# Kernel tuning notes

Measured on AMD Instinct MI355X. Metric: run time of the kernel, lower is better.

Reference implementation:

```python
import jax, jax.numpy as jnp
import numpy as np

H = 768
V = 21128
LN_EPS = 1e-12


def setup_inputs() -> dict:
    key = jax.random.key(0)
    ks = jax.random.split(key, 12)
    s = 0.02
    inp = {
        "cls_vec": jax.random.normal(ks[0], (8, H), dtype=jnp.float32),
        # LSTM (PyTorch layout: weight_ih (4H,H), weight_hh (4H,H), biases (4H,))
        "W_ih": s * jax.random.normal(ks[1], (4 * H, H), dtype=jnp.float32),
        "W_hh": s * jax.random.normal(ks[2], (4 * H, H), dtype=jnp.float32),
        "b_ih": s * jax.random.normal(ks[3], (4 * H,), dtype=jnp.float32),
        "b_hh": s * jax.random.normal(ks[4], (4 * H,), dtype=jnp.float32),
        # BertPredictionHeadTransform: dense(H,H) + gelu + LayerNorm
        "W_dense": s * jax.random.normal(ks[5], (H, H), dtype=jnp.float32),
        "b_dense": s * jax.random.normal(ks[6], (H,), dtype=jnp.float32),
        "ln_gamma": jnp.ones((H,), dtype=jnp.float32),
        "ln_beta": jnp.zeros((H,), dtype=jnp.float32),
        # decoder: Linear(H, V, bias=False) + separate bias param (tied)
        "W_voc": s * jax.random.normal(ks[7], (V, H), dtype=jnp.float32),
        "b_voc": jnp.zeros((V,), dtype=jnp.float32),
        "steps": 511,
    }
    return inp


def _lstm_cell(x, h, c, W_ih, W_hh, b_ih, b_hh):
    gates = x @ W_ih.T + b_ih + h @ W_hh.T + b_hh  # (B, 4H)
    i, f, g, o = jnp.split(gates, 4, axis=-1)
    i = jax.nn.sigmoid(i)
    f = jax.nn.sigmoid(f)
    g = jnp.tanh(g)
    o = jax.nn.sigmoid(o)
    c = f * c + i * g
    h = o * jnp.tanh(c)
    return h, c


def _head(x, W_dense, b_dense, ln_gamma, ln_beta, W_voc, b_voc):
    t = jax.nn.gelu(x @ W_dense.T + b_dense, approximate=False)
    mu = jnp.mean(t, axis=-1, keepdims=True)
    var = jnp.mean(jnp.square(t - mu), axis=-1, keepdims=True)
    t = (t - mu) * jax.lax.rsqrt(var + LN_EPS) * ln_gamma + ln_beta
    return t @ W_voc.T + b_voc  # (B, V)


def reference(cls_vec, W_ih, W_hh, b_ih, b_hh, W_dense, b_dense,
              ln_gamma, ln_beta, W_voc, b_voc, steps):
    B = cls_vec.shape[0]
    zeros = jnp.zeros((B, H), dtype=cls_vec.dtype)
    # decoder_out, (h_1, c_1) = self.decoder(cls_vec.unsqueeze(1))
    h, c = _lstm_cell(cls_vec, zeros, zeros, W_ih, W_hh, b_ih, b_hh)

    def step(carry, _):
        h, c = carry
        h, c = _lstm_cell(carry[0], h, c, W_ih, W_hh, b_ih, b_hh)
        logits = _head(h, W_dense, b_dense, ln_gamma, ln_beta, W_voc, b_voc)
        return (h, c), logits

    (h, c), logits = jax.lax.scan(step, (h, c), None, length=steps)
    return logits  # (steps, B, V)
```

## Files before the change

### kernel.cpp

```cpp
#include <hip/hip_runtime.h>
#include <hip/hip_bf16.h>
#include <cstdint>

#define HD 768
#define VOC 21128
#define VOCP 21248
#define NSTEPS 511
#define MROWS 4088
#define MPAD 4096
#define NBL 192

typedef float f32x4 __attribute__((ext_vector_type(4)));
typedef short short8 __attribute__((ext_vector_type(8)));

#define OFF_HW   768
#define OFF_HALL 49920
#define OFF_WDT  12632576ULL
#define OFF_T    14991872ULL
#define OFF_WV   21283328ULL
#define PADH 772

__device__ __forceinline__ unsigned short f2bf(float x) {
  unsigned u = __float_as_uint(x);
  u += 0x7FFFu + ((u >> 16) & 1u);
  return (unsigned short)(u >> 16);
}

__device__ __forceinline__ void gl_lds16(const void* g, void* l) {
  __builtin_amdgcn_global_load_lds(
      (const __attribute__((address_space(1))) void*)g,
      (__attribute__((address_space(3))) void*)l, 16, 0, 0);
}

__device__ __forceinline__ void st_u32(uint32_t* p, uint32_t v) {
  __hip_atomic_store(p, v, __ATOMIC_RELAXED, __HIP_MEMORY_SCOPE_AGENT);
}
__device__ __forceinline__ uint32_t ld_u32(const uint32_t* p) {
  return __hip_atomic_load(p, __ATOMIC_RELAXED, __HIP_MEMORY_SCOPE_AGENT);
}

__device__ __forceinline__ float swz8(float x) {
  return __int_as_float(__builtin_amdgcn_ds_swizzle(__float_as_int(x), 0x201F));
}
__device__ __forceinline__ float swz16(float x) {
  return __int_as_float(__builtin_amdgcn_ds_swizzle(__float_as_int(x), 0x401F));
}

__device__ __forceinline__ float sigf(float x) {
  return __builtin_amdgcn_rcpf(1.f + __expf(-x));
}
__device__ __forceinline__ float tanhf_fast(float x) {
  float ax = fabsf(x);
  float e = __expf(-2.f * ax);
  float t = (1.f - e) * __builtin_amdgcn_rcpf(1.f + e);
  return copysignf(t, x);
}

__global__ __launch_bounds__(256) void prep_kernel(
    const float* __restrict__ Wd, float* __restrict__ WdT,
    const float* __restrict__ Wv, unsigned short* __restrict__ WvB,
    uint32_t* __restrict__ hw) {
  unsigned idx = blockIdx.x * 256 + threadIdx.x;
  unsigned stride = gridDim.x * 256;
  for (unsigned i = idx; i < 12288; i += stride) hw[i] = 0;
  for (unsigned i = idx; i < HD * HD; i += stride) {
    unsigned k = i / HD, j = i - k * HD;
    WdT[i] = Wd[j * HD + k];
  }
  const unsigned NV = (unsigned)VOCP * HD, NVr = (unsigned)VOC * HD;
  for (unsigned i = idx; i < NV; i += stride)
    WvB[i] = f2bf(i < NVr ? Wv[i] : 0.f);
}

__global__ __launch_bounds__(256) void lstm_kernel(
    const float* __restrict__ cls, const float* __restrict__ Wih,
    const float* __restrict__ Whh, const float* __restrict__ bih,
    const float* __restrict__ bhh, uint32_t* __restrict__ hw,
    float* __restrict__ Hall) {
  __shared__ float h_lds[8 * PADH];
  __shared__ float red[4][2][16][8];
  __shared__ float sbias[16];
  const int t = threadIdx.x;
  const int blk = blockIdx.x;
  const int p_ = t & 7;
  const int s_ = t >> 3;
  const int ks = s_ * 24;
  const int r0 = 2 * p_, r1 = r0 + 1;
  const int grow0 = (r0 >> 2) * HD + blk * 4 + (r0 & 3);
  const int grow1 = (r1 >> 2) * HD + blk * 4 + (r1 & 3);
  float w0[24], w1[24];
#pragma unroll
  for (int j = 0; j < 24; ++j) {
    w0[j] = Wih[(size_t)grow0 * HD + ks + j];
    w1[j] = Wih[(size_t)grow1 * HD + ks + j];
  }
  if (t < 16) {
    int gr = (t >> 2) * HD + blk * 4 + (t & 3);
    sbias[t] = bih[gr] + bhh[gr];
  }
  float cstate = 0.f;
  const int lane = t & 63, wv = t >> 6, hf = (lane >> 5);

  auto do_step = [&](uint32_t* __restrict__ hw_out, int tag,
                     float* __restrict__ hall_row) {
    float acc0[8], acc1[8];
#pragma unroll
    for (int b = 0; b < 8; ++b) { acc0[b] = 0.f; acc1[b] = 0.f; }
#pragma unroll
    for (int b = 0; b < 8; ++b) {
      const float* hb = &h_lds[b * PADH + ks];
#pragma unroll
      for (int j4 = 0; j4 < 6; ++j4) {
        f32x4 hv = *reinterpret_cast<const f32x4*>(hb + j4 * 4);
#pragma unroll
        for (int e = 0; e < 4; ++e) {
          acc0[b] = fmaf(w0[j4 * 4 + e], hv[e], acc0[b]);
          acc1[b] = fmaf(w1[j4 * 4 + e], hv[e], acc1[b]);
        }
      }
    }
#pragma unroll
    for (int b = 0; b < 8; ++b) {
      acc0[b] += swz8(acc0[b]);  acc0[b] += swz16(acc0[b]);
      acc1[b] += swz8(acc1[b]);  acc1[b] += swz16(acc1[b]);
    }
    if ((lane & 31) < 8) {
#pragma unroll
      for (int b = 0; b < 8; ++b) {
        red[wv][hf][r0][b] = acc0[b];
        red[wv][hf][r1][b] = acc1[b];
      }
    }
    __syncthreads();
    if (t < 32) {
      int ul = t >> 3, b = t & 7;
      float gs[4];
#pragma unroll
      for (int g = 0; g < 4; ++g) {
        int r = g * 4 + ul;
        float s = sbias[r];
#pragma unroll
        for (int w2 = 0; w2 < 4; ++w2) s += red[w2][0][r][b] + red[w2][1][r][b];
        gs[g] = s;
      }
      float iv = sigf(gs[0]);
      float fv = sigf(gs[1]);
      float gv = tanhf_fast(gs[2]);
      float ov = sigf(gs[3]);
      cstate = fv * cstate + iv * gv;
      float hn = ov * tanhf_fast(cstate);
      union { _Float16 f; unsigned short u; } cv;
      cv.f = (_Float16)hn;
      st_u32(&hw_out[(blk * 4 + ul) * 8 + b],
             ((uint32_t)tag << 16) | (uint32_t)cv.u);
      if (hall_row) hall_row[(size_t)b * HD + blk * 4 + ul] = hn;
    }
  };

  for (int i = t; i < 1536; i += 256) {
    int b = i / 192, c4 = i - b * 192;
    *reinterpret_cast<f32x4*>(&h_lds[b * PADH + c4 * 4]) =
        reinterpret_cast<const f32x4*>(cls)[i];
  }
  __syncthreads();
  do_step(hw + 6144, 1, nullptr);
#pragma unroll
  for (int j = 0; j < 24; ++j) {
    w0[j] += Whh[(size_t)grow0 * HD + ks + j];
    w1[j] += Whh[(size_t)grow1 * HD + ks + j];
  }
  for (int s = 1; s <= NSTEPS; ++s) {
    const uint32_t* src = hw + (s & 1) * 6144;
    uint32_t w[24];
    bool ok;
    do {
      ok = true;
#pragma unroll
      for (int k = 0; k < 24; ++k) {
        w[k] = ld_u32(&src[t + k * 256]);
        if ((w[k] >> 16) != (uint32_t)s) ok = false;
      }
    } while (!ok);
#pragma unroll
    for (int k = 0; k < 24; ++k) {
      int f = t + k * 256;
      union { unsigned short u; _Float16 f16; } cv;
      cv.u = (unsigned short)(w[k] & 0xFFFFu);
      h_lds[(f & 7) * PADH + (f >> 3)] = (float)cv.f16;
    }
    __syncthreads();
    do_step(hw + ((s + 1) & 1) * 6144, s + 1,
            Hall + (size_t)(s - 1) * (8 * HD));
  }
}

__global__ __launch_bounds__(256) void head_kernel(
    const float* __restrict__ Hall, const float* __restrict__ WdT,
    const float* __restrict__ bd, const float* __restrict__ gamma,
    const float* __restrict__ beta, unsigned short* __restrict__ Tm) {
  __shared__ float hT[HD][16];
  __shared__ float rbuf[4][16];
  __shared__ float mu_s[16], rs_s[16];
  const int t = threadIdx.x;
  const int r0 = blockIdx.x * 16;
  {
    const int row = t & 15, ksl = t >> 4;
    const float* src = Hall + (size_t)(r0 + row) * HD + ksl * 48;
#pragma unroll
    for (int i = 0; i < 12; ++i) {
      f32x4 v = *reinterpret_cast<const f32x4*>(src + i * 4);
      int k = ksl * 48 + i * 4;
      hT[k][row] = v[0]; hT[k + 1][row] = v[1];
      hT[k + 2][row] = v[2]; hT[k + 3][row] = v[3];
    }
  }
  __syncthreads();
  float a0[16], a1[16], a2[16];
#pragma unroll
  for (int r = 0; r < 16; ++r) { a0[r] = 0.f; a1[r] = 0.f; a2[r] = 0.f; }
  for (int k = 0; k < HD; ++k) {
    float wa = WdT[(size_t)k * HD + t];
    float wb = WdT[(size_t)k * HD + t + 256];
    float wc = WdT[(size_t)k * HD + t + 512];
    f32x4 hv4[4];
#pragma unroll
    for (int q = 0; q < 4; ++q)
      hv4[q] = *reinterpret_cast<const f32x4*>(&hT[k][q * 4]);
#pragma unroll
    for (int r = 0; r < 16; ++r) {
      float hv = hv4[r >> 2][r & 3];
      a0[r] = fmaf(wa, hv, a0[r]);
      a1[r] = fmaf(wb, hv, a1[r]);
      a2[r] = fmaf(wc, hv, a2[r]);
    }
  }
  float g0 = gamma[t], g1 = gamma[t + 256], g2 = gamma[t + 512];
  float be0 = beta[t], be1 = beta[t + 256], be2 = beta[t + 512];
  float bd0 = bd[t], bd1 = bd[t + 256], bd2 = bd[t + 512];
#pragma unroll
  for (int r = 0; r < 16; ++r) {
    float x;
    x = a0[r] + bd0; a0[r] = 0.5f * x * (1.f + erff(x * 0.7071067811865476f));
    x = a1[r] + bd1; a1[r] = 0.5f * x * (1.f + erff(x * 0.7071067811865476f));
    x = a2[r] + bd2; a2[r] = 0.5f * x * (1.f + erff(x * 0.7071067811865476f));
  }
  float ps[16];
  const int lane = t & 63, wv = t >> 6;
#pragma unroll
  for (int r = 0; r < 16; ++r) ps[r] = a0[r] + a1[r] + a2[r];
#pragma unroll
  for (int r = 0; r < 16; ++r)
#pragma unroll
    for (int m = 1; m < 64; m <<= 1) ps[r] += __shfl_xor(ps[r], m);
  if (lane == 0) {
#pragma unroll
    for (int r = 0; r < 16; ++r) rbuf[wv][r] = ps[r];
  }
  __syncthreads();
  if (t < 16) mu_s[t] = (rbuf[0][t] + rbuf[1][t] + rbuf[2][t] + rbuf[3][t]) * (1.f / HD);
  __syncthreads();
#pragma unroll
  for (int r = 0; r < 16; ++r) {
    float mu = mu_s[r];
    float d0 = a0[r] - mu, d1 = a1[r] - mu, d2 = a2[r] - mu;
    ps[r] = d0 * d0 + d1 * d1 + d2 * d2;
  }
#pragma unroll
  for (int r = 0; r < 16; ++r)
#pragma unroll
    for (int m = 1; m < 64; m <<= 1) ps[r] += __shfl_xor(ps[r], m);
  if (lane == 0) {
#pragma unroll
    for (int r = 0; r < 16; ++r) rbuf[wv][r] = ps[r];
  }
  __syncthreads();
  if (t < 16)
    rs_s[t] = 1.f / sqrtf((rbuf[0][t] + rbuf[1][t] + rbuf[2][t] + rbuf[3][t]) * (1.f / HD) + 1e-12f);
  __syncthreads();
#pragma unroll
  for (int r = 0; r < 16; ++r) {
    float mu = mu_s[r], rs = rs_s[r];
    size_t ro = (size_t)(r0 + r) * HD;
    Tm[ro + t]       = f2bf((a0[r] - mu) * rs * g0 + be0);
    Tm[ro + t + 256] = f2bf((a1[r] - mu) * rs * g1 + be1);
    Tm[ro + t + 512] = f2bf((a2[r] - mu) * rs * g2 + be2);
  }
}

__global__ __launch_bounds__(256) void gemm_kernel(
    const unsigned short* __restrict__ Tm, const unsigned short* __restrict__ Wv,
    const float* __restrict__ bvoc, float* __restrict__ out) {
  __shared__ unsigned short As[128 * 64];
  __shared__ unsigned short Bs[128 * 64];
  const int t = threadIdx.x;
  const int lane = t & 63, wid = t >> 6;
  const int wm = wid >> 1, wn = wid & 1;
  const int nbx = VOCP / 128;
  int lid = blockIdx.y * nbx + blockIdx.x;
  int swz = (lid & 7) * ((nbx * (MPAD / 128)) >> 3) + (lid >> 3);
  const int m0 = (swz / nbx) * 128, n0 = (swz % nbx) * 128;
  const int lrow = lane & 15, lgrp = lane >> 4;
  f32x4 acc[4][4] = {};
  for (int kt = 0; kt < HD; kt += 64) {
#pragma unroll
    for (int it = 0; it < 4; ++it) {
      int slot = it * 256 + t;
      int row = slot >> 3, g = slot & 7;
      int sg = g ^ (row & 7);
      const unsigned short* sa = Tm + (size_t)(m0 + row) * HD + kt + sg * 8;
      const unsigned short* sb = Wv + (size_t)(n0 + row) * HD + kt + sg * 8;
      unsigned short* da = &As[(it * 256 + wid * 64) * 8];
      unsigned short* db = &Bs[(it * 256 + wid * 64) * 8];
      gl_lds16(sa, da);
      gl_lds16(sb, db);
    }
    __syncthreads();
#pragma unroll
    for (int kk = 0; kk < 2; ++kk) {
      short8 af[4], bfr[4];
#pragma unroll
      for (int i = 0; i < 4; ++i) {
        int row = wm * 64 + i * 16 + lrow;
        int gg = (kk * 4 + lgrp) ^ (row & 7);
        af[i] = *reinterpret_cast<const short8*>(&As[row * 64 + gg * 8]);
      }
#pragma unroll
      for (int j = 0; j < 4; ++j) {
        int row = wn * 64 + j * 16 + lrow;
        int gg = (kk * 4 + lgrp) ^ (row & 7);
        bfr[j] = *reinterpret_cast<const short8*>(&Bs[row * 64 + gg * 8]);
      }
#pragma unroll
      for (int i = 0; i < 4; ++i)
#pragma unroll
        for (int j = 0; j < 4; ++j)
          acc[i][j] = __builtin_amdgcn_mfma_f32_16x16x32_bf16(af[i], bfr[j], acc[i][j], 0, 0, 0);
    }
    __syncthreads();
  }
#pragma unroll
  for (int j = 0; j < 4; ++j) {
    int col = n0 + wn * 64 + j * 16 + lrow;
    bool cok = col < VOC;
    float bv = cok ? bvoc[col] : 0.f;
#pragma unroll
    for (int i = 0; i < 4; ++i) {
      int rbase = m0 + wm * 64 + i * 16 + lgrp * 4;
#pragma unroll
      for (int e = 0; e < 4; ++e) {
        int row = rbase + e;
        if (cok && row < MROWS) out[(size_t)row * VOC + col] = acc[i][j][e] + bv;
      }
    }
  }
}

extern "C" void kernel_launch(void* const* d_in, const int* in_sizes, int n_in,
                              void* d_out, int out_size, void* d_ws, size_t ws_size,
                              hipStream_t stream) {
  (void)in_sizes; (void)n_in; (void)out_size; (void)ws_size;
  const float* cls  = (const float*)d_in[0];
  const float* Wih  = (const float*)d_in[1];
  const float* Whh  = (const float*)d_in[2];
  const float* bih  = (const float*)d_in[3];
  const float* bhh  = (const float*)d_in[4];
  const float* Wd   = (const float*)d_in[5];
  const float* bd   = (const float*)d_in[6];
  const float* gmm  = (const float*)d_in[7];
  const float* bet  = (const float*)d_in[8];
  const float* Wv   = (const float*)d_in[9];
  const float* bvoc = (const float*)d_in[10];
  char* ws = (char*)d_ws;
  uint32_t* hw   = (uint32_t*)(ws + OFF_HW);
  float* Hall  = (float*)(ws + OFF_HALL);
  float* WdT   = (float*)(ws + OFF_WDT);
  unsigned short* Tm  = (unsigned short*)(ws + OFF_T);
  unsigned short* WvB = (unsigned short*)(ws + OFF_WV);
  float* out = (float*)d_out;

  hipLaunchKernelGGL(prep_kernel, dim3(4096), dim3(256), 0, stream, Wd, WdT, Wv, WvB, hw);
  hipLaunchKernelGGL(lstm_kernel, dim3(NBL), dim3(256), 0, stream,
                     cls, Wih, Whh, bih, bhh, hw, Hall);
  hipLaunchKernelGGL(head_kernel, dim3(MPAD / 16), dim3(256), 0, stream,
                     Hall, WdT, bd, gmm, bet, Tm);
  hipLaunchKernelGGL(gemm_kernel, dim3(VOCP / 128, MPAD / 128), dim3(256), 0, stream,
                     Tm, WvB, bvoc, out);
}
```

Measured before the change: 2.158 ms.

## Move head dense projection to bf16 MFMA GEMM and split LayerNorm kernel

Replaces the fp32 FMA head kernel with a bf16 MFMA tiled GEMM that fuses bias and GELU. A separate kernel then applies LayerNorm in place. The LSTM now writes its hidden states as bf16, and the prep step converts W_dense to bf16 instead of transposing it in fp32. The goal is to cut the cost of the scalar fp32 dense matmul over 4088 rows. In exchange it loses precision by rounding hidden states and the pre-LN activations to bf16, and adds one extra kernel launch plus a round trip through global memory.

```diff
diff --git a/kernel.cpp b/kernel.cpp
--- a/kernel.cpp
+++ b/kernel.cpp
@@ -13,17 +13,20 @@
 typedef float f32x4 __attribute__((ext_vector_type(4)));
 typedef short short8 __attribute__((ext_vector_type(8)));
 
-#define OFF_HW   768
-#define OFF_HALL 49920
-#define OFF_WDT  12632576ULL
-#define OFF_T    14991872ULL
-#define OFF_WV   21283328ULL
+#define OFF_HW    768
+#define OFF_HALLB 49920ULL
+#define OFF_DT    6341376ULL
+#define OFF_WDB   12632832ULL
+#define OFF_WV    13812480ULL
 #define PADH 772
 
 __device__ __forceinline__ unsigned short f2bf(float x) {
   unsigned u = __float_as_uint(x);
   u += 0x7FFFu + ((u >> 16) & 1u);
   return (unsigned short)(u >> 16);
+}
+__device__ __forceinline__ float bf2f(unsigned short u) {
+  return __uint_as_float(((unsigned)u) << 16);
 }
 
 __device__ __forceinline__ void gl_lds16(const void* g, void* l) {
@@ -57,16 +60,13 @@
 }
 
 __global__ __launch_bounds__(256) void prep_kernel(
-    const float* __restrict__ Wd, float* __restrict__ WdT,
+    const float* __restrict__ Wd, unsigned short* __restrict__ WdB,
     const float* __restrict__ Wv, unsigned short* __restrict__ WvB,
     uint32_t* __restrict__ hw) {
   unsigned idx = blockIdx.x * 256 + threadIdx.x;
   unsigned stride = gridDim.x * 256;
   for (unsigned i = idx; i < 12288; i += stride) hw[i] = 0;
-  for (unsigned i = idx; i < HD * HD; i += stride) {
-    unsigned k = i / HD, j = i - k * HD;
-    WdT[i] = Wd[j * HD + k];
-  }
+  for (unsigned i = idx; i < HD * HD; i += stride) WdB[i] = f2bf(Wd[i]);
   const unsigned NV = (unsigned)VOCP * HD, NVr = (unsigned)VOC * HD;
   for (unsigned i = idx; i < NV; i += stride)
     WvB[i] = f2bf(i < NVr ? Wv[i] : 0.f);
@@ -76,7 +76,7 @@
     const float* __restrict__ cls, const float* __restrict__ Wih,
     const float* __restrict__ Whh, const float* __restrict__ bih,
     const float* __restrict__ bhh, uint32_t* __restrict__ hw,
-    float* __restrict__ Hall) {
+    unsigned short* __restrict__ HallB) {
   __shared__ float h_lds[8 * PADH];
   __shared__ float red[4][2][16][8];
   __shared__ float sbias[16];
@@ -102,7 +102,7 @@
   const int lane = t & 63, wv = t >> 6, hf = (lane >> 5);
 
   auto do_step = [&](uint32_t* __restrict__ hw_out, int tag,
-                     float* __restrict__ hall_row) {
+                     unsigned short* __restrict__ hall_row) {
     float acc0[8], acc1[8];
 #pragma unroll
     for (int b = 0; b < 8; ++b) { acc0[b] = 0.f; acc1[b] = 0.f; }
@@ -153,7 +153,7 @@
       cv.f = (_Float16)hn;
       st_u32(&hw_out[(blk * 4 + ul) * 8 + b],
              ((uint32_t)tag << 16) | (uint32_t)cv.u);
-      if (hall_row) hall_row[(size_t)b * HD + blk * 4 + ul] = hn;
+      if (hall_row) hall_row[(size_t)b * HD + blk * 4 + ul] = f2bf(hn);
     }
   };
 
@@ -190,60 +190,95 @@
     }
     __syncthreads();
     do_step(hw + ((s + 1) & 1) * 6144, s + 1,
-            Hall + (size_t)(s - 1) * (8 * HD));
-  }
-}
-
-__global__ __launch_bounds__(256) void head_kernel(
-    const float* __restrict__ Hall, const float* __restrict__ WdT,
-    const float* __restrict__ bd, const float* __restrict__ gamma,
-    const float* __restrict__ beta, unsigned short* __restrict__ Tm) {
-  __shared__ float hT[HD][16];
+            HallB + (size_t)(s - 1) * (8 * HD));
+  }
+}
+
+__global__ __launch_bounds__(256) void head_mm_kernel(
+    const unsigned short* __restrict__ Ha, const unsigned short* __restrict__ Wb,
+    const float* __restrict__ bd, unsigned short* __restrict__ DT) {
+  __shared__ unsigned short As[128 * 64];
+  __shared__ unsigned short Bs[128 * 64];
+  const int t = threadIdx.x;
+  const int lane = t & 63, wid = t >> 6;
+  const int wm = wid >> 1, wn = wid & 1;
+  const int m0 = blockIdx.y * 128, n0 = blockIdx.x * 128;
+  const int lrow = lane & 15, lgrp = lane >> 4;
+  f32x4 acc[4][4] = {};
+  for (int kt = 0; kt < HD; kt += 64) {
+#pragma unroll
+    for (int it = 0; it < 4; ++it) {
+      int slot = it * 256 + t;
+      int row = slot >> 3, g = slot & 7;
+      int sg = g ^ (row & 7);
+      const unsigned short* sa = Ha + (size_t)(m0 + row) * HD + kt + sg * 8;
+      const unsigned short* sb = Wb + (size_t)(n0 + row) * HD + kt + sg * 8;
+      unsigned short* da = &As[(it * 256 + wid * 64) * 8];
+      unsigned short* db = &Bs[(it * 256 + wid * 64) * 8];
+      gl_lds16(sa, da);
+      gl_lds16(sb, db);
+    }
+    __syncthreads();
+#pragma unroll
+    for (int kk = 0; kk < 2; ++kk) {
+      short8 af[4], bfr[4];
+#pragma unroll
+      for (int i = 0; i < 4; ++i) {
+        int row = wm * 64 + i * 16 + lrow;
+        int gg = (kk * 4 + lgrp) ^ (row & 7);
+        af[i] = *reinterpret_cast<const short8*>(&As[row * 64 + gg * 8]);
+      }
+#pragma unroll
+      for (int j = 0; j < 4; ++j) {
+        int row = wn * 64 + j * 16 + lrow;
+        int gg = (kk * 4 + lgrp) ^ (row & 7);
+        bfr[j] = *reinterpret_cast<const short8*>(&Bs[row * 64 + gg * 8]);
+      }
+#pragma unroll
+      for (int i = 0; i < 4; ++i)
+#pragma unroll
+        for (int j = 0; j < 4; ++j)
+          acc[i][j] = __builtin_amdgcn_mfma_f32_16x16x32_bf16(af[i], bfr[j], acc[i][j], 0, 0, 0);
+    }
+    __syncthreads();
+  }
+#pragma unroll
+  for (int j = 0; j < 4; ++j) {
+    int col = n0 + wn * 64 + j * 16 + lrow;
+    float bv = bd[col];
+#pragma unroll
+    for (int i = 0; i < 4; ++i) {
+      int rbase = m0 + wm * 64 + i * 16 + lgrp * 4;
+#pragma unroll
+      for (int e = 0; e < 4; ++e) {
+        int row = rbase + e;
+        if (row < MROWS) {
+          float x = acc[i][j][e] + bv;
+          float g = 0.5f * x * (1.f + erff(x * 0.7071067811865476f));
+          DT[(size_t)row * HD + col] = f2bf(g);
+        }
+      }
+    }
+  }
+}
+
+__global__ __launch_bounds__(256) void ln_kernel(
+    unsigned short* __restrict__ DT, const float* __restrict__ gamma,
+    const float* __restrict__ beta) {
   __shared__ float rbuf[4][16];
   __shared__ float mu_s[16], rs_s[16];
   const int t = threadIdx.x;
   const int r0 = blockIdx.x * 16;
-  {
-    const int row = t & 15, ksl = t >> 4;
-    const float* src = Hall + (size_t)(r0 + row) * HD + ksl * 48;
-#pragma unroll
-    for (int i = 0; i < 12; ++i) {
-      f32x4 v = *reinterpret_cast<const f32x4*>(src + i * 4);
-      int k = ksl * 48 + i * 4;
-      hT[k][row] = v[0]; hT[k + 1][row] = v[1];
-      hT[k + 2][row] = v[2]; hT[k + 3][row] = v[3];
-    }
-  }
-  __syncthreads();
   float a0[16], a1[16], a2[16];
 #pragma unroll
-  for (int r = 0; r < 16; ++r) { a0[r] = 0.f; a1[r] = 0.f; a2[r] = 0.f; }
-  for (int k = 0; k < HD; ++k) {
-    float wa = WdT[(size_t)k * HD + t];
-    float wb = WdT[(size_t)k * HD + t + 256];
-    float wc = WdT[(size_t)k * HD + t + 512];
-    f32x4 hv4[4];
-#pragma unroll
-    for (int q = 0; q < 4; ++q)
-      hv4[q] = *reinterpret_cast<const f32x4*>(&hT[k][q * 4]);
-#pragma unroll
-    for (int r = 0; r < 16; ++r) {
-      float hv = hv4[r >> 2][r & 3];
-      a0[r] = fmaf(wa, hv, a0[r]);
-      a1[r] = fmaf(wb, hv, a1[r]);
-      a2[r] = fmaf(wc, hv, a2[r]);
-    }
+  for (int r = 0; r < 16; ++r) {
+    size_t ro = (size_t)(r0 + r) * HD;
+    a0[r] = bf2f(DT[ro + t]);
+    a1[r] = bf2f(DT[ro + t + 256]);
+    a2[r] = bf2f(DT[ro + t + 512]);
   }
   float g0 = gamma[t], g1 = gamma[t + 256], g2 = gamma[t + 512];
   float be0 = beta[t], be1 = beta[t + 256], be2 = beta[t + 512];
-  float bd0 = bd[t], bd1 = bd[t + 256], bd2 = bd[t + 512];
-#pragma unroll
-  for (int r = 0; r < 16; ++r) {
-    float x;
-    x = a0[r] + bd0; a0[r] = 0.5f * x * (1.f + erff(x * 0.7071067811865476f));
-    x = a1[r] + bd1; a1[r] = 0.5f * x * (1.f + erff(x * 0.7071067811865476f));
-    x = a2[r] + bd2; a2[r] = 0.5f * x * (1.f + erff(x * 0.7071067811865476f));
-  }
   float ps[16];
   const int lane = t & 63, wv = t >> 6;
 #pragma unroll
@@ -281,9 +316,9 @@
   for (int r = 0; r < 16; ++r) {
     float mu = mu_s[r], rs = rs_s[r];
     size_t ro = (size_t)(r0 + r) * HD;
-    Tm[ro + t]       = f2bf((a0[r] - mu) * rs * g0 + be0);
-    Tm[ro + t + 256] = f2bf((a1[r] - mu) * rs * g1 + be1);
-    Tm[ro + t + 512] = f2bf((a2[r] - mu) * rs * g2 + be2);
+    DT[ro + t]       = f2bf((a0[r] - mu) * rs * g0 + be0);
+    DT[ro + t + 256] = f2bf((a1[r] - mu) * rs * g1 + be1);
+    DT[ro + t + 512] = f2bf((a2[r] - mu) * rs * g2 + be2);
   }
 }
 
@@ -371,18 +406,20 @@
   const float* Wv   = (const float*)d_in[9];
   const float* bvoc = (const float*)d_in[10];
   char* ws = (char*)d_ws;
-  uint32_t* hw   = (uint32_t*)(ws + OFF_HW);
-  float* Hall  = (float*)(ws + OFF_HALL);
-  float* WdT   = (float*)(ws + OFF_WDT);
-  unsigned short* Tm  = (unsigned short*)(ws + OFF_T);
-  unsigned short* WvB = (unsigned short*)(ws + OFF_WV);
+  uint32_t* hw = (uint32_t*)(ws + OFF_HW);
+  unsigned short* HallB = (unsigned short*)(ws + OFF_HALLB);
+  unsigned short* DT    = (unsigned short*)(ws + OFF_DT);
+  unsigned short* WdB   = (unsigned short*)(ws + OFF_WDB);
+  unsigned short* WvB   = (unsigned short*)(ws + OFF_WV);
   float* out = (float*)d_out;
 
-  hipLaunchKernelGGL(prep_kernel, dim3(4096), dim3(256), 0, stream, Wd, WdT, Wv, WvB, hw);
+  hipLaunchKernelGGL(prep_kernel, dim3(4096), dim3(256), 0, stream, Wd, WdB, Wv, WvB, hw);
   hipLaunchKernelGGL(lstm_kernel, dim3(NBL), dim3(256), 0, stream,
-                     cls, Wih, Whh, bih, bhh, hw, Hall);
-  hipLaunchKernelGGL(head_kernel, dim3(MPAD / 16), dim3(256), 0, stream,
-                     Hall, WdT, bd, gmm, bet, Tm);
+                     cls, Wih, Whh, bih, bhh, hw, HallB);
+  hipLaunchKernelGGL(head_mm_kernel, dim3(HD / 128, MPAD / 128), dim3(256), 0, stream,
+                     HallB, WdB, bd, DT);
+  hipLaunchKernelGGL(ln_kernel, dim3(MPAD / 16), dim3(256), 0, stream,
+                     DT, gmm, bet);
   hipLaunchKernelGGL(gemm_kernel, dim3(VOCP / 128, MPAD / 128), dim3(256), 0, stream,
-                     Tm, WvB, bvoc, out);
-}
+                     DT, WvB, bvoc, out);
+}
```

Measured after the change: 2.068 ms. 4.1% less time.
